# Kernel tuning notes

Measured on AMD Instinct MI355X. Metric: run time of the kernel, lower is better.

## Reference

```python
import jax, jax.numpy as jnp
import numpy as np

B, S, D, H = 4, 2048, 1024, 16
DH = D // H


def setup_inputs() -> dict:
    key = jax.random.key(0)
    ks = jax.random.split(key, 11)
    s = 1.0 / np.sqrt(D)
    return {
        "query": jax.random.normal(ks[0], (B, S, D), jnp.float32),
        "key": jax.random.normal(ks[1], (B, S, D), jnp.float32),
        "value": jax.random.normal(ks[2], (B, S, D), jnp.float32),
        "Wq": jax.random.normal(ks[3], (D, D), jnp.float32) * s,
        "bq": jnp.zeros((D,), jnp.float32),
        "Wk": jax.random.normal(ks[4], (D, D), jnp.float32) * s,
        "bk": jnp.zeros((D,), jnp.float32),
        "Wv": jax.random.normal(ks[5], (D, D), jnp.float32) * s,
        "bv": jnp.zeros((D,), jnp.float32),
        "Wo": jax.random.normal(ks[6], (D, D), jnp.float32) * s,
        "bo": jnp.zeros((D,), jnp.float32),
    }


def reference(query, key, value, Wq, bq, Wk, bk, Wv, bv, Wo, bo):
    # QKV projections (nn.Linear: x @ W.T + b; here W stored as [in, out])
    q = (query @ Wq + bq).reshape(B, S, H, DH).transpose(0, 2, 1, 3)  # [B,H,S,DH]
    k = (key @ Wk + bk).reshape(B, S, H, DH).transpose(0, 2, 1, 3)
    v = (value @ Wv + bv).reshape(B, S, H, DH).transpose(0, 2, 1, 3)
    # scaled dot-product attention (dropout in eval mode -> identity)
    scores = jnp.einsum("bhqd,bhkd->bhqk", q, k) / jnp.sqrt(jnp.float32(DH))
    attn = jax.nn.softmax(scores, axis=-1)
    out = jnp.einsum("bhqk,bhkd->bhqd", attn, v)  # [B,H,S,DH]
    out = out.transpose(0, 2, 1, 3).reshape(B, S, D)
    return out @ Wo + bo
```

## Files before the change

kernel.cpp:

```cpp
#include <hip/hip_runtime.h>


typedef __bf16 bf16x8 __attribute__((ext_vector_type(8)));
typedef __bf16 bf16x4 __attribute__((ext_vector_type(4)));
typedef float f32x4 __attribute__((ext_vector_type(4)));

#define GLAS __attribute__((address_space(1)))
#define LDSAS __attribute__((address_space(3)))

__device__ __forceinline__ void gl16(const void* g, void* l) {
  __builtin_amdgcn_global_load_lds((GLAS void*)const_cast<void*>(g),
                                   (LDSAS void*)l, 16, 0, 0);
}

__global__ __launch_bounds__(256) void wt_cvt(const float* __restrict__ w,
                                              __bf16* __restrict__ wt, float scl) {
  __shared__ float t[32][33];
  const int n0 = blockIdx.x * 32, k0 = blockIdx.y * 32;
  const int x = threadIdx.x, y = threadIdx.y;
#pragma unroll
  for (int i = 0; i < 32; i += 8) t[y + i][x] = w[(k0 + y + i) * 1024 + n0 + x];
  __syncthreads();
#pragma unroll
  for (int i = 0; i < 32; i += 8)
    wt[(n0 + y + i) * 1024 + (k0 + x)] = (__bf16)(t[x][y + i] * scl);
}

__global__ __launch_bounds__(256) void cvt_k(const float* __restrict__ in,
                                             __bf16* __restrict__ out) {
  const int i = (blockIdx.x * 256 + threadIdx.x) * 8;
  const float4 f0 = *(const float4*)(in + i);
  const float4 f1 = *(const float4*)(in + i + 4);
  bf16x8 o;
  o[0] = (__bf16)f0.x; o[1] = (__bf16)f0.y; o[2] = (__bf16)f0.z; o[3] = (__bf16)f0.w;
  o[4] = (__bf16)f1.x; o[5] = (__bf16)f1.y; o[6] = (__bf16)f1.z; o[7] = (__bf16)f1.w;
  *(bf16x8*)(out + i) = o;
}

template <int MODE>
__global__ __launch_bounds__(256) void gemm_k(const __bf16* __restrict__ A,
                                              const __bf16* __restrict__ BT,
                                              const float* __restrict__ bias, float bsc,
                                              void* __restrict__ outp) {
  __shared__ __align__(16) char smem[32768];
  const int tid = threadIdx.x, wid = tid >> 6, lane = tid & 63;
  const int wr = wid >> 1, wc = wid & 1;
  const int m0 = blockIdx.y * 128, n0 = blockIdx.x * 128;
  const int lr = lane & 15, lg = lane >> 4;

  const int srow = lane >> 3;
  const int scl8 = (lane & 7) ^ srow;
  const __bf16* Ab = A + (m0 + wid * 32 + srow) * 1024 + scl8 * 8;
  const __bf16* Bb = BT + (n0 + wid * 32 + srow) * 1024 + scl8 * 8;
  char* AsW = smem + wid * 4096;
  char* BsW = smem + 16384 + wid * 4096;

  f32x4 acc[4][4] = {};

  for (int k0 = 0; k0 < 1024; k0 += 64) {
#pragma unroll
    for (int i = 0; i < 4; ++i) {
      gl16(Ab + i * 8192 + k0, AsW + i * 1024);
      gl16(Bb + i * 8192 + k0, BsW + i * 1024);
    }
    __syncthreads();
#pragma unroll
    for (int ks = 0; ks < 2; ++ks) {
      bf16x8 af[4], bfv[4];
      const int co = (ks * 64 + lg * 16) ^ ((lr & 7) << 4);
#pragma unroll
      for (int i = 0; i < 4; ++i) {
        af[i]  = *(const bf16x8*)(smem + (wr * 64 + i * 16 + lr) * 128 + co);
        bfv[i] = *(const bf16x8*)(smem + 16384 + (wc * 64 + i * 16 + lr) * 128 + co);
      }
#pragma unroll
      for (int i = 0; i < 4; ++i)
#pragma unroll
        for (int j = 0; j < 4; ++j)
          acc[i][j] = __builtin_amdgcn_mfma_f32_16x16x32_bf16(af[i], bfv[j], acc[i][j], 0, 0, 0);
    }
    __syncthreads();
  }

#pragma unroll
  for (int i = 0; i < 4; ++i)
#pragma unroll
    for (int j = 0; j < 4; ++j) {
      const int n = n0 + wc * 64 + j * 16 + lr;
      const float bb = bias[n] * bsc;
#pragma unroll
      for (int r = 0; r < 4; ++r) {
        const int m = m0 + wr * 64 + i * 16 + lg * 4 + r;
        const float v = acc[i][j][r] + bb;
        if (MODE == 2) {
          ((float*)outp)[m * 1024 + n] = v;
        } else {
          const int b = m >> 11, s = m & 2047;
          const int h = n >> 6, dh = n & 63;
          if (MODE == 0)
            ((__bf16*)outp)[(((b * 16 + h) * 2048 + s) << 6) + dh] = (__bf16)v;
          else
            ((__bf16*)outp)[(((b * 16 + h) * 64 + dh) << 11) + s] = (__bf16)v;
        }
      }
    }
}

__global__ __launch_bounds__(256) void attn_k(const __bf16* __restrict__ Qp,
                                              const __bf16* __restrict__ Kp,
                                              const __bf16* __restrict__ Vt,
                                              __bf16* __restrict__ ctx) {
  __shared__ __align__(16) char smem[40960];
  const int tid = threadIdx.x, wid = tid >> 6, lane = tid & 63;
  const int lr = lane & 15, lg = lane >> 4;
  const int bh = blockIdx.y;
  const int q0 = blockIdx.x * 64 + wid * 16;
  const int S = 2048;

  const int srow = lane >> 3;
  const int scl8 = (lane & 7) ^ srow;
  const __bf16* Kbase = Kp + (bh * S + srow) * 64 + scl8 * 8;
  const __bf16* Vbase = Vt + (bh * 64 + srow) * S + scl8 * 8;
  char* Ps = smem + 32768 + wid * 2048;

  bf16x8 aq[2];
#pragma unroll
  for (int ks = 0; ks < 2; ++ks)
    aq[ks] = *(const bf16x8*)(Qp + (bh * S + q0 + lr) * 64 + ks * 32 + lg * 8);

  float m_run = -1e30f, l_run = 0.f;
  f32x4 acc_o[4] = {};

#pragma unroll
  for (int i = 0; i < 2; ++i) {
    const int ch = wid * 2 + i;
    gl16(Kbase + ch * 512, smem + ch * 1024);
    gl16(Vbase + ch * 16384, smem + 16384 + ch * 1024);
  }

  int cur = 0;
  for (int t = 0; t < 32; ++t) {
    __syncthreads();
    if (t + 1 < 32) {
      const int kv1 = (t + 1) * 64;
      char* Kd = smem + (cur ^ 1) * 8192;
      char* Vd = smem + 16384 + (cur ^ 1) * 8192;
#pragma unroll
      for (int i = 0; i < 2; ++i) {
        const int ch = wid * 2 + i;
        gl16(Kbase + kv1 * 64 + ch * 512, Kd + ch * 1024);
        gl16(Vbase + kv1 + ch * 16384, Vd + ch * 1024);
      }
    }
    const char* Ks = smem + cur * 8192;
    const char* Vs = smem + 16384 + cur * 8192;

    f32x4 sc[4] = {};
    __builtin_amdgcn_s_setprio(1);
#pragma unroll
    for (int cb = 0; cb < 4; ++cb) {
#pragma unroll
      for (int ks = 0; ks < 2; ++ks) {
        const int krow = cb * 16 + lr;
        const bf16x8 kf = *(const bf16x8*)(Ks + krow * 128 +
                                           ((ks * 64 + lg * 16) ^ ((krow & 7) << 4)));
        sc[cb] = __builtin_amdgcn_mfma_f32_16x16x32_bf16(kf, aq[ks], sc[cb], 0, 0, 0);
      }
    }
    __builtin_amdgcn_s_setprio(0);

    float mx = sc[0][0];
#pragma unroll
    for (int cb = 0; cb < 4; ++cb)
#pragma unroll
      for (int r = 0; r < 4; ++r) mx = fmaxf(mx, sc[cb][r]);
    mx = fmaxf(mx, __shfl_xor(mx, 16, 64));
    mx = fmaxf(mx, __shfl_xor(mx, 32, 64));
    const float mnew = fmaxf(m_run, mx);
    const float corr = __builtin_amdgcn_exp2f(m_run - mnew);
    m_run = mnew;
    float rs = 0.f;
#pragma unroll
    for (int cb = 0; cb < 4; ++cb) {
      bf16x4 pk;
#pragma unroll
      for (int r = 0; r < 4; ++r) {
        const float p = __builtin_amdgcn_exp2f(sc[cb][r] - mnew);
        rs += p;
        pk[r] = (__bf16)p;
      }
      *(bf16x4*)(Ps + lr * 128 + ((cb * 32 + lg * 8) ^ ((lr & 7) << 4))) = pk;
    }
    rs += __shfl_xor(rs, 16, 64);
    rs += __shfl_xor(rs, 32, 64);
    l_run = l_run * corr + rs;
    float corrv[4];
#pragma unroll
    for (int r = 0; r < 4; ++r) corrv[r] = __shfl(corr, lg * 4 + r, 64);
#pragma unroll
    for (int dhb = 0; dhb < 4; ++dhb)
#pragma unroll
      for (int r = 0; r < 4; ++r) acc_o[dhb][r] *= corrv[r];

    bf16x8 pa[2];
#pragma unroll
    for (int ks = 0; ks < 2; ++ks)
      pa[ks] = *(const bf16x8*)(Ps + lr * 128 + ((ks * 64 + lg * 16) ^ ((lr & 7) << 4)));
    __builtin_amdgcn_s_setprio(1);
#pragma unroll
    for (int dhb = 0; dhb < 4; ++dhb) {
#pragma unroll
      for (int ks = 0; ks < 2; ++ks) {
        const int vrow = dhb * 16 + lr;
        const bf16x8 vf = *(const bf16x8*)(Vs + vrow * 128 +
                                           ((ks * 64 + lg * 16) ^ ((vrow & 7) << 4)));
        acc_o[dhb] = __builtin_amdgcn_mfma_f32_16x16x32_bf16(pa[ks], vf, acc_o[dhb], 0, 0, 0);
      }
    }
    __builtin_amdgcn_s_setprio(0);
    cur ^= 1;
  }

  const int b = bh >> 4, h = bh & 15;
  float linv[4];
#pragma unroll
  for (int r = 0; r < 4; ++r) linv[r] = 1.f / __shfl(l_run, lg * 4 + r, 64);
#pragma unroll
  for (int dhb = 0; dhb < 4; ++dhb)
#pragma unroll
    for (int r = 0; r < 4; ++r) {
      const int sr = q0 + lg * 4 + r;
      const int d = h * 64 + dhb * 16 + lr;
      ctx[(b * 2048 + sr) * 1024 + d] = (__bf16)(acc_o[dhb][r] * linv[r]);
    }
}

extern "C" void kernel_launch(void* const* d_in, const int* in_sizes, int n_in,
                              void* d_out, int out_size, void* d_ws, size_t ws_size,
                              hipStream_t stream) {
  const float* query = (const float*)d_in[0];
  const float* key   = (const float*)d_in[1];
  const float* value = (const float*)d_in[2];
  const float* Wq = (const float*)d_in[3];
  const float* bq = (const float*)d_in[4];
  const float* Wk = (const float*)d_in[5];
  const float* bk = (const float*)d_in[6];
  const float* Wv = (const float*)d_in[7];
  const float* bv = (const float*)d_in[8];
  const float* Wo = (const float*)d_in[9];
  const float* bo = (const float*)d_in[10];

  char* ws = (char*)d_ws;
  __bf16* WqT = (__bf16*)(ws + 0 * 2097152);
  __bf16* WkT = (__bf16*)(ws + 1 * 2097152);
  __bf16* WvT = (__bf16*)(ws + 2 * 2097152);
  __bf16* WoT = (__bf16*)(ws + 3 * 2097152);
  __bf16* Abf = (__bf16*)(ws + 8388608);
  __bf16* Qp  = (__bf16*)(ws + 25165824);
  __bf16* Kp  = (__bf16*)(ws + 41943040);
  __bf16* Vt  = (__bf16*)(ws + 58720256);
  __bf16* ctx = Abf;

  const float SCL = 0.125f * 1.44269504088896340736f;

  const dim3 tb(32, 8);
  wt_cvt<<<dim3(32, 32), tb, 0, stream>>>(Wq, WqT, SCL);
  wt_cvt<<<dim3(32, 32), tb, 0, stream>>>(Wk, WkT, 1.f);
  wt_cvt<<<dim3(32, 32), tb, 0, stream>>>(Wv, WvT, 1.f);
  wt_cvt<<<dim3(32, 32), tb, 0, stream>>>(Wo, WoT, 1.f);

  const dim3 gg(8, 64);
  cvt_k<<<4096, 256, 0, stream>>>(query, Abf);
  gemm_k<0><<<gg, 256, 0, stream>>>(Abf, WqT, bq, SCL, Qp);
  cvt_k<<<4096, 256, 0, stream>>>(key, Abf);
  gemm_k<0><<<gg, 256, 0, stream>>>(Abf, WkT, bk, 1.f, Kp);
  cvt_k<<<4096, 256, 0, stream>>>(value, Abf);
  gemm_k<1><<<gg, 256, 0, stream>>>(Abf, WvT, bv, 1.f, Vt);

  attn_k<<<dim3(32, 64), 256, 0, stream>>>(Qp, Kp, Vt, ctx);

  gemm_k<2><<<gg, 256, 0, stream>>>(ctx, WoT, bo, 1.f, (float*)d_out);
}
```

Before: 398.3 us.

## Batch QKV projections into one launch and double query rows per attention wave

The three QKV projection GEMMs now run as a single launch over a 3x larger grid, with separate activation buffers so all three conversions finish first. This fills the device better and removes launch gaps. The attention kernel has each wave handle two 16-row query tiles against every K/V tile loaded to LDS, so each K/V fragment read is reused twice and the grid is halved. In exchange it uses more registers, may lower occupancy, and leaves fewer blocks in the attention grid.

```diff
diff --git a/kernel.cpp b/kernel.cpp
--- a/kernel.cpp
+++ b/kernel.cpp
@@ -37,11 +37,81 @@
   *(bf16x8*)(out + i) = o;
 }
 
-template <int MODE>
-__global__ __launch_bounds__(256) void gemm_k(const __bf16* __restrict__ A,
+__global__ __launch_bounds__(256) void gemm_qkv(
+    const __bf16* __restrict__ Abase, const __bf16* __restrict__ Wbase,
+    const float* __restrict__ bq, const float* __restrict__ bk,
+    const float* __restrict__ bv, float sclq,
+    __bf16* __restrict__ Qp, __bf16* __restrict__ Kp, __bf16* __restrict__ Vtp) {
+  __shared__ __align__(16) char smem[32768];
+  const int tid = threadIdx.x, wid = tid >> 6, lane = tid & 63;
+  const int wr = wid >> 1, wc = wid & 1;
+  const int sel = blockIdx.y >> 6;
+  const int m0 = (blockIdx.y & 63) * 128, n0 = blockIdx.x * 128;
+  const int lr = lane & 15, lg = lane >> 4;
+
+  const int srow = lane >> 3;
+  const int scl8 = (lane & 7) ^ srow;
+  const __bf16* A  = Abase + sel * 8388608;
+  const __bf16* BT = Wbase + sel * 1048576;
+  const __bf16* Ab = A + (m0 + wid * 32 + srow) * 1024 + scl8 * 8;
+  const __bf16* Bb = BT + (n0 + wid * 32 + srow) * 1024 + scl8 * 8;
+  char* AsW = smem + wid * 4096;
+  char* BsW = smem + 16384 + wid * 4096;
+
+  f32x4 acc[4][4] = {};
+
+  for (int k0 = 0; k0 < 1024; k0 += 64) {
+#pragma unroll
+    for (int i = 0; i < 4; ++i) {
+      gl16(Ab + i * 8192 + k0, AsW + i * 1024);
+      gl16(Bb + i * 8192 + k0, BsW + i * 1024);
+    }
+    __syncthreads();
+#pragma unroll
+    for (int ks = 0; ks < 2; ++ks) {
+      bf16x8 af[4], bfv[4];
+      const int co = (ks * 64 + lg * 16) ^ ((lr & 7) << 4);
+#pragma unroll
+      for (int i = 0; i < 4; ++i) {
+        af[i]  = *(const bf16x8*)(smem + (wr * 64 + i * 16 + lr) * 128 + co);
+        bfv[i] = *(const bf16x8*)(smem + 16384 + (wc * 64 + i * 16 + lr) * 128 + co);
+      }
+#pragma unroll
+      for (int i = 0; i < 4; ++i)
+#pragma unroll
+        for (int j = 0; j < 4; ++j)
+          acc[i][j] = __builtin_amdgcn_mfma_f32_16x16x32_bf16(af[i], bfv[j], acc[i][j], 0, 0, 0);
+    }
+    __syncthreads();
+  }
+
+  const float* bias = sel == 0 ? bq : (sel == 1 ? bk : bv);
+  const float bsc = sel == 0 ? sclq : 1.f;
+  __bf16* outp = sel == 0 ? Qp : (sel == 1 ? Kp : Vtp);
+#pragma unroll
+  for (int i = 0; i < 4; ++i)
+#pragma unroll
+    for (int j = 0; j < 4; ++j) {
+      const int n = n0 + wc * 64 + j * 16 + lr;
+      const float bb = bias[n] * bsc;
+#pragma unroll
+      for (int r = 0; r < 4; ++r) {
+        const int m = m0 + wr * 64 + i * 16 + lg * 4 + r;
+        const float v = acc[i][j][r] + bb;
+        const int b = m >> 11, s = m & 2047;
+        const int h = n >> 6, dh = n & 63;
+        if (sel < 2)
+          outp[(((b * 16 + h) * 2048 + s) << 6) + dh] = (__bf16)v;
+        else
+          outp[(((b * 16 + h) * 64 + dh) << 11) + s] = (__bf16)v;
+      }
+    }
+}
+
+__global__ __launch_bounds__(256) void gemm_o(const __bf16* __restrict__ A,
                                               const __bf16* __restrict__ BT,
-                                              const float* __restrict__ bias, float bsc,
-                                              void* __restrict__ outp) {
+                                              const float* __restrict__ bias,
+                                              float* __restrict__ outp) {
   __shared__ __align__(16) char smem[32768];
   const int tid = threadIdx.x, wid = tid >> 6, lane = tid & 63;
   const int wr = wid >> 1, wc = wid & 1;
@@ -87,21 +157,11 @@
 #pragma unroll
     for (int j = 0; j < 4; ++j) {
       const int n = n0 + wc * 64 + j * 16 + lr;
-      const float bb = bias[n] * bsc;
+      const float bb = bias[n];
 #pragma unroll
       for (int r = 0; r < 4; ++r) {
         const int m = m0 + wr * 64 + i * 16 + lg * 4 + r;
-        const float v = acc[i][j][r] + bb;
-        if (MODE == 2) {
-          ((float*)outp)[m * 1024 + n] = v;
-        } else {
-          const int b = m >> 11, s = m & 2047;
-          const int h = n >> 6, dh = n & 63;
-          if (MODE == 0)
-            ((__bf16*)outp)[(((b * 16 + h) * 2048 + s) << 6) + dh] = (__bf16)v;
-          else
-            ((__bf16*)outp)[(((b * 16 + h) * 64 + dh) << 11) + s] = (__bf16)v;
-        }
+        outp[m * 1024 + n] = acc[i][j][r] + bb;
       }
     }
 }
@@ -114,7 +174,7 @@
   const int tid = threadIdx.x, wid = tid >> 6, lane = tid & 63;
   const int lr = lane & 15, lg = lane >> 4;
   const int bh = blockIdx.y;
-  const int q0 = blockIdx.x * 64 + wid * 16;
+  const int q0 = blockIdx.x * 128 + wid * 32;
   const int S = 2048;
 
   const int srow = lane >> 3;
@@ -123,13 +183,16 @@
   const __bf16* Vbase = Vt + (bh * 64 + srow) * S + scl8 * 8;
   char* Ps = smem + 32768 + wid * 2048;
 
-  bf16x8 aq[2];
-#pragma unroll
-  for (int ks = 0; ks < 2; ++ks)
-    aq[ks] = *(const bf16x8*)(Qp + (bh * S + q0 + lr) * 64 + ks * 32 + lg * 8);
-
-  float m_run = -1e30f, l_run = 0.f;
-  f32x4 acc_o[4] = {};
+  bf16x8 aq[2][2];
+#pragma unroll
+  for (int qs = 0; qs < 2; ++qs)
+#pragma unroll
+    for (int ks = 0; ks < 2; ++ks)
+      aq[qs][ks] = *(const bf16x8*)(Qp + (bh * S + q0 + qs * 16 + lr) * 64 +
+                                    ks * 32 + lg * 8);
+
+  float m_run[2] = {-1e30f, -1e30f}, l_run[2] = {0.f, 0.f};
+  f32x4 acc_o[2][4] = {};
 
 #pragma unroll
   for (int i = 0; i < 2; ++i) {
@@ -155,7 +218,7 @@
     const char* Ks = smem + cur * 8192;
     const char* Vs = smem + 16384 + cur * 8192;
 
-    f32x4 sc[4] = {};
+    f32x4 sc[2][4] = {};
     __builtin_amdgcn_s_setprio(1);
 #pragma unroll
     for (int cb = 0; cb < 4; ++cb) {
@@ -164,48 +227,53 @@
         const int krow = cb * 16 + lr;
         const bf16x8 kf = *(const bf16x8*)(Ks + krow * 128 +
                                            ((ks * 64 + lg * 16) ^ ((krow & 7) << 4)));
-        sc[cb] = __builtin_amdgcn_mfma_f32_16x16x32_bf16(kf, aq[ks], sc[cb], 0, 0, 0);
+        sc[0][cb] = __builtin_amdgcn_mfma_f32_16x16x32_bf16(kf, aq[0][ks], sc[0][cb], 0, 0, 0);
+        sc[1][cb] = __builtin_amdgcn_mfma_f32_16x16x32_bf16(kf, aq[1][ks], sc[1][cb], 0, 0, 0);
       }
     }
     __builtin_amdgcn_s_setprio(0);
 
-    float mx = sc[0][0];
-#pragma unroll
-    for (int cb = 0; cb < 4; ++cb)
-#pragma unroll
-      for (int r = 0; r < 4; ++r) mx = fmaxf(mx, sc[cb][r]);
-    mx = fmaxf(mx, __shfl_xor(mx, 16, 64));
-    mx = fmaxf(mx, __shfl_xor(mx, 32, 64));
-    const float mnew = fmaxf(m_run, mx);
-    const float corr = __builtin_amdgcn_exp2f(m_run - mnew);
-    m_run = mnew;
-    float rs = 0.f;
-#pragma unroll
-    for (int cb = 0; cb < 4; ++cb) {
-      bf16x4 pk;
-#pragma unroll
-      for (int r = 0; r < 4; ++r) {
-        const float p = __builtin_amdgcn_exp2f(sc[cb][r] - mnew);
-        rs += p;
-        pk[r] = (__bf16)p;
-      }
-      *(bf16x4*)(Ps + lr * 128 + ((cb * 32 + lg * 8) ^ ((lr & 7) << 4))) = pk;
-    }
-    rs += __shfl_xor(rs, 16, 64);
-    rs += __shfl_xor(rs, 32, 64);
-    l_run = l_run * corr + rs;
-    float corrv[4];
-#pragma unroll
-    for (int r = 0; r < 4; ++r) corrv[r] = __shfl(corr, lg * 4 + r, 64);
-#pragma unroll
-    for (int dhb = 0; dhb < 4; ++dhb)
-#pragma unroll
-      for (int r = 0; r < 4; ++r) acc_o[dhb][r] *= corrv[r];
-
-    bf16x8 pa[2];
-#pragma unroll
-    for (int ks = 0; ks < 2; ++ks)
-      pa[ks] = *(const bf16x8*)(Ps + lr * 128 + ((ks * 64 + lg * 16) ^ ((lr & 7) << 4)));
+    bf16x8 pa[2][2];
+#pragma unroll
+    for (int qs = 0; qs < 2; ++qs) {
+      float mx = sc[qs][0][0];
+#pragma unroll
+      for (int cb = 0; cb < 4; ++cb)
+#pragma unroll
+        for (int r = 0; r < 4; ++r) mx = fmaxf(mx, sc[qs][cb][r]);
+      mx = fmaxf(mx, __shfl_xor(mx, 16, 64));
+      mx = fmaxf(mx, __shfl_xor(mx, 32, 64));
+      const float mnew = fmaxf(m_run[qs], mx);
+      const float corr = __builtin_amdgcn_exp2f(m_run[qs] - mnew);
+      m_run[qs] = mnew;
+      float rs = 0.f;
+#pragma unroll
+      for (int cb = 0; cb < 4; ++cb) {
+        bf16x4 pk;
+#pragma unroll
+        for (int r = 0; r < 4; ++r) {
+          const float p = __builtin_amdgcn_exp2f(sc[qs][cb][r] - mnew);
+          rs += p;
+          pk[r] = (__bf16)p;
+        }
+        *(bf16x4*)(Ps + lr * 128 + ((cb * 32 + lg * 8) ^ ((lr & 7) << 4))) = pk;
+      }
+      rs += __shfl_xor(rs, 16, 64);
+      rs += __shfl_xor(rs, 32, 64);
+      l_run[qs] = l_run[qs] * corr + rs;
+      float corrv[4];
+#pragma unroll
+      for (int r = 0; r < 4; ++r) corrv[r] = __shfl(corr, lg * 4 + r, 64);
+#pragma unroll
+      for (int dhb = 0; dhb < 4; ++dhb)
+#pragma unroll
+        for (int r = 0; r < 4; ++r) acc_o[qs][dhb][r] *= corrv[r];
+#pragma unroll
+      for (int ks = 0; ks < 2; ++ks)
+        pa[qs][ks] = *(const bf16x8*)(Ps + lr * 128 +
+                                      ((ks * 64 + lg * 16) ^ ((lr & 7) << 4)));
+    }
+
     __builtin_amdgcn_s_setprio(1);
 #pragma unroll
     for (int dhb = 0; dhb < 4; ++dhb) {
@@ -214,7 +282,8 @@
         const int vrow = dhb * 16 + lr;
         const bf16x8 vf = *(const bf16x8*)(Vs + vrow * 128 +
                                            ((ks * 64 + lg * 16) ^ ((vrow & 7) << 4)));
-        acc_o[dhb] = __builtin_amdgcn_mfma_f32_16x16x32_bf16(pa[ks], vf, acc_o[dhb], 0, 0, 0);
+        acc_o[0][dhb] = __builtin_amdgcn_mfma_f32_16x16x32_bf16(pa[0][ks], vf, acc_o[0][dhb], 0, 0, 0);
+        acc_o[1][dhb] = __builtin_amdgcn_mfma_f32_16x16x32_bf16(pa[1][ks], vf, acc_o[1][dhb], 0, 0, 0);
       }
     }
     __builtin_amdgcn_s_setprio(0);
@@ -222,17 +291,20 @@
   }
 
   const int b = bh >> 4, h = bh & 15;
-  float linv[4];
-#pragma unroll
-  for (int r = 0; r < 4; ++r) linv[r] = 1.f / __shfl(l_run, lg * 4 + r, 64);
-#pragma unroll
-  for (int dhb = 0; dhb < 4; ++dhb)
-#pragma unroll
-    for (int r = 0; r < 4; ++r) {
-      const int sr = q0 + lg * 4 + r;
-      const int d = h * 64 + dhb * 16 + lr;
-      ctx[(b * 2048 + sr) * 1024 + d] = (__bf16)(acc_o[dhb][r] * linv[r]);
-    }
+#pragma unroll
+  for (int qs = 0; qs < 2; ++qs) {
+    float linv[4];
+#pragma unroll
+    for (int r = 0; r < 4; ++r) linv[r] = 1.f / __shfl(l_run[qs], lg * 4 + r, 64);
+#pragma unroll
+    for (int dhb = 0; dhb < 4; ++dhb)
+#pragma unroll
+      for (int r = 0; r < 4; ++r) {
+        const int sr = q0 + qs * 16 + lg * 4 + r;
+        const int d = h * 64 + dhb * 16 + lr;
+        ctx[(b * 2048 + sr) * 1024 + d] = (__bf16)(acc_o[qs][dhb][r] * linv[r]);
+      }
+  }
 }
 
 extern "C" void kernel_launch(void* const* d_in, const int* in_sizes, int n_in,
@@ -251,33 +323,30 @@
   const float* bo = (const float*)d_in[10];
 
   char* ws = (char*)d_ws;
-  __bf16* WqT = (__bf16*)(ws + 0 * 2097152);
-  __bf16* WkT = (__bf16*)(ws + 1 * 2097152);
-  __bf16* WvT = (__bf16*)(ws + 2 * 2097152);
-  __bf16* WoT = (__bf16*)(ws + 3 * 2097152);
-  __bf16* Abf = (__bf16*)(ws + 8388608);
-  __bf16* Qp  = (__bf16*)(ws + 25165824);
-  __bf16* Kp  = (__bf16*)(ws + 41943040);
-  __bf16* Vt  = (__bf16*)(ws + 58720256);
-  __bf16* ctx = Abf;
+  const size_t MiB = 1048576;
+  __bf16* Wqkv = (__bf16*)(ws);
+  __bf16* WoT  = (__bf16*)(ws + 6 * MiB);
+  __bf16* Abf  = (__bf16*)(ws + 8 * MiB);
+  __bf16* Qp   = (__bf16*)(ws + 56 * MiB);
+  __bf16* Kp   = (__bf16*)(ws + 72 * MiB);
+  __bf16* Vt   = (__bf16*)(ws + 88 * MiB);
+  __bf16* ctx  = Abf;
 
   const float SCL = 0.125f * 1.44269504088896340736f;
 
   const dim3 tb(32, 8);
-  wt_cvt<<<dim3(32, 32), tb, 0, stream>>>(Wq, WqT, SCL);
-  wt_cvt<<<dim3(32, 32), tb, 0, stream>>>(Wk, WkT, 1.f);
-  wt_cvt<<<dim3(32, 32), tb, 0, stream>>>(Wv, WvT, 1.f);
-  wt_cvt<<<dim3(32, 32), tb, 0, stream>>>(Wo, WoT, 1.f);
-
-  const dim3 gg(8, 64);
+  wt_cvt<<<dim3(32, 32), tb, 0, stream>>>(Wq, Wqkv,              SCL);
+  wt_cvt<<<dim3(32, 32), tb, 0, stream>>>(Wk, Wqkv + 1048576,    1.f);
+  wt_cvt<<<dim3(32, 32), tb, 0, stream>>>(Wv, Wqkv + 2097152,    1.f);
+  wt_cvt<<<dim3(32, 32), tb, 0, stream>>>(Wo, WoT,               1.f);
+
   cvt_k<<<4096, 256, 0, stream>>>(query, Abf);
-  gemm_k<0><<<gg, 256, 0, stream>>>(Abf, WqT, bq, SCL, Qp);
-  cvt_k<<<4096, 256, 0, stream>>>(key, Abf);
-  gemm_k<0><<<gg, 256, 0, stream>>>(Abf, WkT, bk, 1.f, Kp);
-  cvt_k<<<4096, 256, 0, stream>>>(value, Abf);
-  gemm_k<1><<<gg, 256, 0, stream>>>(Abf, WvT, bv, 1.f, Vt);
-
-  attn_k<<<dim3(32, 64), 256, 0, stream>>>(Qp, Kp, Vt, ctx);
-
-  gemm_k<2><<<gg, 256, 0, stream>>>(ctx, WoT, bo, 1.f, (float*)d_out);
-}
+  cvt_k<<<4096, 256, 0, stream>>>(key,   Abf + 8388608);
+  cvt_k<<<4096, 256, 0, stream>>>(value, Abf + 16777216);
+
+  gemm_qkv<<<dim3(8, 192), 256, 0, stream>>>(Abf, Wqkv, bq, bk, bv, SCL, Qp, Kp, Vt);
+
+  attn_k<<<dim3(16, 64), 256, 0, stream>>>(Qp, Kp, Vt, ctx);
+
+  gemm_o<<<dim3(8, 64), 256, 0, stream>>>(ctx, WoT, bo, (float*)d_out);
+}
```

New measurement: 415.6 us. +4.3%, slower.
